# Optimization experiments

Measured on AMD Instinct MI355X. Metric: run time of the kernel, lower is better.

The kernel has to match this reference:

```python
import jax, jax.numpy as jnp
import numpy as np

SP, WD, H, HID = 8, 3, 8, 256
D = HID // H
TEMP = 0.1


def setup_inputs() -> dict:
    key = jax.random.key(0)
    ks = jax.random.split(key, 14)
    B, Lq, Lk, F = 4, 1024, 2048, SP + WD
    s = 0.05
    return {
        "q_fp": jax.random.normal(ks[0], (B, Lq, F), jnp.float32),
        "v_ret": jax.random.normal(ks[1], (B, Lk, F), jnp.float32),
        "pi_star": jax.random.uniform(ks[2], (B, Lq, Lk), jnp.float32),
        "Wq_s": jax.random.normal(ks[3], (HID, SP), jnp.float32) * s,
        "bq_s": jax.random.normal(ks[4], (HID,), jnp.float32) * s,
        "Wk_s": jax.random.normal(ks[5], (HID, SP), jnp.float32) * s,
        "bk_s": jax.random.normal(ks[6], (HID,), jnp.float32) * s,
        "Wq_w": jax.random.normal(ks[7], (HID, WD), jnp.float32) * s,
        "bq_w": jax.random.normal(ks[8], (HID,), jnp.float32) * s,
        "Wk_w": jax.random.normal(ks[9], (HID, WD), jnp.float32) * s,
        "bk_w": jax.random.normal(ks[10], (HID,), jnp.float32) * s,
        "Wv": jax.random.normal(ks[11], (HID, F), jnp.float32) * s,
        "bv": jnp.zeros((HID,), jnp.float32),
        "Wo": jax.random.normal(ks[12], (HID, HID), jnp.float32) * s,
        "bo": jnp.zeros((HID,), jnp.float32),
        "wave_blend": jnp.array(0.5, jnp.float32),
    }


def _proj(x, W, b):
    # x: [B, L, F_in] -> [B, H, L, D]
    B, L, _ = x.shape
    return (x @ W.T + b).reshape(B, L, H, D).transpose(0, 2, 1, 3)


def reference(q_fp, v_ret, pi_star, Wq_s, bq_s, Wk_s, bk_s, Wq_w, bq_w, Wk_w, bk_w, Wv, bv, Wo, bo, wave_blend):
    B, Lq, _ = q_fp.shape
    # split streams: first SP dims spatial, next WD dims wave (F == SP+WD)
    q_sp, q_wv = q_fp[..., :SP], q_fp[..., SP:SP + WD]
    k_sp, k_wv = v_ret[..., :SP], v_ret[..., SP:SP + WD]
    # structural branch: scaled dot product
    q_struct = _proj(q_sp, Wq_s, bq_s)
    k_struct = _proj(k_sp, Wk_s, bk_s)
    spatial_logits = jnp.einsum('bhqd,bhkd->bhqk', q_struct, k_struct) / np.float32(np.sqrt(D))
    # wave branch: negative squared euclidean distance via norm expansion
    q_wp = _proj(q_wv, Wq_w, bq_w)
    k_wp = _proj(k_wv, Wk_w, bk_w)
    qn = jnp.sum(q_wp * q_wp, axis=-1)[..., :, None]   # [B,H,Lq,1]
    kn = jnp.sum(k_wp * k_wp, axis=-1)[..., None, :]   # [B,H,1,Lk]
    qk = jnp.einsum('bhqd,bhkd->bhqk', q_wp, k_wp)
    wave_logits = -(qn + kn - 2.0 * qk) / np.float32(TEMP)
    alpha = jax.nn.sigmoid(wave_blend)
    transport_mask = jnp.log(jnp.clip(pi_star, 1e-9, None))[:, None]  # [B,1,Lq,Lk]
    attn = jax.nn.softmax((1.0 - alpha) * spatial_logits + alpha * wave_logits + transport_mask, axis=-1)
    values = _proj(v_ret, Wv, bv)  # [B,H,Lk,D]
    ctx = jnp.einsum('bhqk,bhkd->bhqd', attn, values)
    ctx = ctx.transpose(0, 2, 1, 3).reshape(B, Lq, HID)
    return ctx @ Wo.T + bo
```

## Files before the change

### kernel.cpp

```cpp
#include <hip/hip_runtime.h>
#include <hip/hip_bf16.h>
#include <cstdint>

#define B_    4
#define LQ    1024
#define LK    2048
#define FEAT  11
#define SP_   8
#define WD_   3
#define H_    8
#define HID_  256
#define LOG2E 1.4426950408889634f
#define SPLIT 2
#define KPS   (LK / SPLIT)
#define ITERS (KPS / 64)

typedef __attribute__((ext_vector_type(4))) float f32x4;
typedef __attribute__((ext_vector_type(8))) short bf16x8;

__device__ __forceinline__ float sigmoidf_(float x) { return 1.f / (1.f + __expf(-x)); }

__device__ __forceinline__ short f2bf(float f) {
  unsigned u = __float_as_uint(f);
  u += 0x7fffu + ((u >> 16) & 1u);
  return (short)(u >> 16);
}

__device__ __forceinline__ void gl_lds16(const void* g, void* l) {
  __builtin_amdgcn_global_load_lds(
      (const __attribute__((address_space(1))) unsigned int*)g,
      (__attribute__((address_space(3))) unsigned int*)l, 16, 0, 0);
}

__global__ __launch_bounds__(256) void proj_q_kernel(
    const float* __restrict__ q_fp, const float* __restrict__ Wq_s,
    const float* __restrict__ bq_s, const float* __restrict__ Wq_w,
    const float* __restrict__ bq_w, const float* __restrict__ wb,
    short* __restrict__ Qh)
{
  const int row = blockIdx.x;
  const int t   = threadIdx.x;
  const float alpha = sigmoidf_(wb[0]);
  const float c1 = (1.f - alpha) * 0.17677669529663687f * LOG2E;
  const float c2 = 2.f * alpha * 10.f * LOG2E;

  const float* x = q_fp + (size_t)row * FEAT;
  float xs[FEAT];
  #pragma unroll
  for (int f = 0; f < FEAT; ++f) xs[f] = x[f];

  float s = bq_s[t];
  #pragma unroll
  for (int f = 0; f < SP_; ++f) s += xs[f] * Wq_s[t * SP_ + f];
  float w = bq_w[t];
  #pragma unroll
  for (int f = 0; f < WD_; ++f) w += xs[SP_ + f] * Wq_w[t * WD_ + f];

  const int h = t >> 5, d = t & 31;
  const int b = row >> 10, q = row & (LQ - 1);
  const size_t base = ((size_t)(b * H_ + h) * LQ + q) * 64;
  Qh[base + d]      = f2bf(c1 * s);
  Qh[base + 32 + d] = f2bf(c2 * w);
}

__global__ __launch_bounds__(256) void projk_pack_kernel(
    const float* __restrict__ v_ret, const float* __restrict__ Wk_s,
    const float* __restrict__ bk_s, const float* __restrict__ Wk_w,
    const float* __restrict__ bk_w, const float* __restrict__ Wv,
    const float* __restrict__ bv,   const float* __restrict__ wb,
    short* __restrict__ KV, float* __restrict__ kb)
{
  __shared__ float ldsv[64][33];
  const int blk = blockIdx.x, bh = blockIdx.y;
  const int b = bh >> 3, h = bh & 7;
  const int t = threadIdx.x;
  const int kl = t >> 2, part = t & 3;
  const int k = blk * 64 + kl;
  const float alpha = sigmoidf_(wb[0]);

  const float* x = v_ret + (size_t)(b * LK + k) * FEAT;
  float xs[FEAT];
  #pragma unroll
  for (int f = 0; f < FEAT; ++f) xs[f] = x[f];

  float s8[8], w8[8], v8[8];
  #pragma unroll
  for (int i = 0; i < 8; ++i) {
    const int d = h * 32 + part * 8 + i;
    float s = bk_s[d];
    #pragma unroll
    for (int f = 0; f < SP_; ++f) s += xs[f] * Wk_s[d * SP_ + f];
    float w = bk_w[d];
    #pragma unroll
    for (int f = 0; f < WD_; ++f) w += xs[SP_ + f] * Wk_w[d * WD_ + f];
    float v = bv[d];
    #pragma unroll
    for (int f = 0; f < FEAT; ++f) v += xs[f] * Wv[d * FEAT + f];
    s8[i] = s; w8[i] = w; v8[i] = v;
    ldsv[kl][part * 8 + i] = v;
  }

  float sq = 0.f;
  #pragma unroll
  for (int i = 0; i < 8; ++i) sq += w8[i] * w8[i];
  sq += __shfl_xor(sq, 1);
  sq += __shfl_xor(sq, 2);
  if (part == 0) kb[(size_t)bh * LK + k] = -10.f * alpha * LOG2E * sq;

  const int a  = kl >> 5;
  const int bb = (kl >> 2) & 1;
  const int p  = kl - a * 32 - bb * 4;
  const int lo = ((p >> 3) << 2) | (p & 3);
  const int t4 = a * 2 + bb;
  const size_t base = ((size_t)bh * 32 + blk) * 768;

  bf16x8 hs, hw;
  #pragma unroll
  for (int i = 0; i < 8; ++i) { hs[i] = f2bf(s8[i]); hw[i] = f2bf(w8[i]); }
  *(bf16x8*)(KV + (base + (t4 * 2 + 0) * 64 + part * 16 + lo) * 8) = hs;
  *(bf16x8*)(KV + (base + (t4 * 2 + 1) * 64 + part * 16 + lo) * 8) = hw;

  __syncthreads();

  {
    const int j = t >> 6, l = t & 63;
    const int dt = j >> 1, kw = j & 1;
    const int lo2 = l & 15, quad = l >> 4;
    const int d = dt * 16 + lo2;
    bf16x8 hv;
    #pragma unroll
    for (int i = 0; i < 8; ++i)
      hv[i] = f2bf(ldsv[kw * 32 + quad * 8 + i][d]);
    *(bf16x8*)(KV + (base + 512 + t) * 8) = hv;
  }
}

__global__ __launch_bounds__(256) void pi_prepack_kernel(
    const float* __restrict__ pi, float* __restrict__ piP)
{
  const int Gid = blockIdx.x * 256 + threadIdx.x;
  const int g    = Gid & 255;
  const int kblk = (Gid >> 8) & 31;
  const int qt   = (Gid >> 13) & 63;
  const int b    = Gid >> 19;
  const int t4 = g >> 6, l = g & 63;
  const int lo = l & 15, quad = l >> 4;
  const int q = qt * 16 + lo;
  const int k = kblk * 64 + ((t4 >> 1) << 5) + ((t4 & 1) << 2) + quad * 8;
  const f32x4 v = *(const f32x4*)(pi + ((size_t)(b * LQ + q) * LK + k));
  *(f32x4*)(piP + (size_t)Gid * 4) = v;
}

union PF { int i[4]; bf16x8 v; };

__global__ __launch_bounds__(256, 4) void attn_kernel(
    const short* __restrict__ Qh, const short* __restrict__ KV,
    const float* __restrict__ kb, const float* __restrict__ piP,
    float* __restrict__ part)
{
  __shared__ short skv[2][6144];
  const int bh = blockIdx.y;
  const int sp = blockIdx.z;
  const int b = bh >> 3;
  const int wv = threadIdx.x >> 6;
  const int lane = threadIdx.x & 63;
  const int lo16 = lane & 15;
  const int quad = lane >> 4;
  const int q = blockIdx.x * 64 + wv * 16 + lo16;
  const int qt = blockIdx.x * 4 + wv;
  const int k0 = sp * KPS;
  const int blk0 = sp * 16;

  const size_t qoff = ((size_t)bh * LQ + q) * 64 + quad * 8;
  const bf16x8 qh0 = *(const bf16x8*)(Qh + qoff);
  const bf16x8 qh1 = *(const bf16x8*)(Qh + qoff + 32);

  const float* pibase = piP + (((size_t)(b * 64 + qt) * 32 + blk0) << 10) + lane * 4;
  const float* kbbase = kb + (size_t)bh * LK + k0 + quad * 8;

  float m = -1e30f, l = 0.f;
  f32x4 o0 = {0.f, 0.f, 0.f, 0.f}, o1 = {0.f, 0.f, 0.f, 0.f};

  {
    const size_t gb = ((size_t)bh * 32 + blk0) * 768;
    #pragma unroll
    for (int c = 0; c < 3; ++c)
      gl_lds16(KV + (gb + c * 256 + wv * 64 + lane) * 8,
               &skv[0][c * 2048 + wv * 512]);
  }

  #pragma unroll 2
  for (int it = 0; it < ITERS; ++it) {
    __syncthreads();
    if (it + 1 < ITERS) {
      const size_t gb = ((size_t)bh * 32 + blk0 + it + 1) * 768;
      short* db = skv[(it + 1) & 1];
      #pragma unroll
      for (int c = 0; c < 3; ++c)
        gl_lds16(KV + (gb + c * 256 + wv * 64 + lane) * 8,
                 db + c * 2048 + wv * 512);
    }
    const short* cbuf = skv[it & 1];

    const float* pp = pibase + (it << 10);
    f32x4 pi4[4];
    #pragma unroll
    for (int t4 = 0; t4 < 4; ++t4) pi4[t4] = *(const f32x4*)(pp + t4 * 256);
    const float* bp = kbbase + it * 64;
    f32x4 kb4[4];
    kb4[0] = *(const f32x4*)(bp);      kb4[1] = *(const f32x4*)(bp + 4);
    kb4[2] = *(const f32x4*)(bp + 32); kb4[3] = *(const f32x4*)(bp + 36);

    f32x4 st[4];
    #pragma unroll
    for (int t4 = 0; t4 < 4; ++t4) {
      const bf16x8 ka0 = *(const bf16x8*)(cbuf + ((t4 * 2 + 0) * 64 + lane) * 8);
      const bf16x8 ka1 = *(const bf16x8*)(cbuf + ((t4 * 2 + 1) * 64 + lane) * 8);
      f32x4 z = {0.f, 0.f, 0.f, 0.f};
      z = __builtin_amdgcn_mfma_f32_16x16x32_bf16(ka0, qh0, z, 0, 0, 0);
      z = __builtin_amdgcn_mfma_f32_16x16x32_bf16(ka1, qh1, z, 0, 0, 0);
      st[t4] = z;
    }

    float lg[16];
    #pragma unroll
    for (int t4 = 0; t4 < 4; ++t4) {
      #pragma unroll
      for (int r = 0; r < 4; ++r) lg[t4 * 4 + r] = st[t4][r] + kb4[t4][r];
    }

    float cm = lg[0];
    #pragma unroll
    for (int j = 1; j < 16; ++j) cm = fmaxf(cm, lg[j]);
    cm = fmaxf(cm, __shfl_xor(cm, 16));
    cm = fmaxf(cm, __shfl_xor(cm, 32));
    const float mn = fmaxf(m, cm);
    const float sc = __builtin_amdgcn_exp2f(m - mn);

    unsigned eu[16];
    #pragma unroll
    for (int t4 = 0; t4 < 4; ++t4) {
      #pragma unroll
      for (int r = 0; r < 4; ++r)
        eu[t4 * 4 + r] = __float_as_uint(
            __builtin_amdgcn_exp2f(lg[t4 * 4 + r] - mn) * fmaxf(pi4[t4][r], 1e-9f));
    }

    PF pf0, pf1;
    float ps = 0.f;
    #pragma unroll
    for (int p = 0; p < 4; ++p) {
      const int w0 = __builtin_amdgcn_perm(eu[2 * p + 1], eu[2 * p], 0x07060302u);
      const int w1 = __builtin_amdgcn_perm(eu[8 + 2 * p + 1], eu[8 + 2 * p], 0x07060302u);
      pf0.i[p] = w0; pf1.i[p] = w1;
      ps += __uint_as_float(((unsigned)w0) << 16) + __uint_as_float(w0 & 0xffff0000u);
      ps += __uint_as_float(((unsigned)w1) << 16) + __uint_as_float(w1 & 0xffff0000u);
    }
    ps += __shfl_xor(ps, 16);
    ps += __shfl_xor(ps, 32);
    l = l * sc + ps;
    m = mn;
    #pragma unroll
    for (int r = 0; r < 4; ++r) { o0[r] *= sc; o1[r] *= sc; }

    const bf16x8 va00 = *(const bf16x8*)(cbuf + ((512 + 0 * 64) + lane) * 8);
    const bf16x8 va01 = *(const bf16x8*)(cbuf + ((512 + 1 * 64) + lane) * 8);
    const bf16x8 va10 = *(const bf16x8*)(cbuf + ((512 + 2 * 64) + lane) * 8);
    const bf16x8 va11 = *(const bf16x8*)(cbuf + ((512 + 3 * 64) + lane) * 8);
    o0 = __builtin_amdgcn_mfma_f32_16x16x32_bf16(va00, pf0.v, o0, 0, 0, 0);
    o0 = __builtin_amdgcn_mfma_f32_16x16x32_bf16(va01, pf1.v, o0, 0, 0, 0);
    o1 = __builtin_amdgcn_mfma_f32_16x16x32_bf16(va10, pf0.v, o1, 0, 0, 0);
    o1 = __builtin_amdgcn_mfma_f32_16x16x32_bf16(va11, pf1.v, o1, 0, 0, 0);
  }

  float* ppart = part + ((size_t)(sp * 32 + bh) * LQ + q) * 36;
  if (quad == 0) { ppart[0] = m; ppart[1] = l; }
  *(f32x4*)(ppart + 4 + quad * 4)  = o0;
  *(f32x4*)(ppart + 20 + quad * 4) = o1;
}

__global__ __launch_bounds__(256) void out_kernel(
    const float* __restrict__ part, const float* __restrict__ Wo,
    const float* __restrict__ bo, float* __restrict__ out)
{
  __shared__ float cs[16 * 256];
  const int t = threadIdx.x;
  const size_t r0 = (size_t)blockIdx.x * 16;

  {
    const int col4 = (t & 63) * 4;
    const int h = col4 >> 5, d = col4 & 31;
    #pragma unroll
    for (int i = 0; i < 4; ++i) {
      const int row = i * 4 + (t >> 6);
      const size_t gq = r0 + row;
      const int b = (int)(gq >> 10), qq = (int)(gq & (LQ - 1));
      const size_t r = ((size_t)(b * H_ + h) * LQ + qq);
      const float* p0 = part + r * 36;
      const float* p1 = part + (r + (size_t)B_ * H_ * LQ) * 36;
      const float m0 = p0[0], l0 = p0[1], m1 = p1[0], l1 = p1[1];
      const float mM = fmaxf(m0, m1);
      const float w0 = __builtin_amdgcn_exp2f(m0 - mM);
      const float w1 = __builtin_amdgcn_exp2f(m1 - mM);
      const float inv = 1.f / (w0 * l0 + w1 * l1);
      const f32x4 a0 = *(const f32x4*)(p0 + 4 + d);
      const f32x4 a1 = *(const f32x4*)(p1 + 4 + d);
      f32x4 cv;
      #pragma unroll
      for (int j = 0; j < 4; ++j) cv[j] = (w0 * a0[j] + w1 * a1[j]) * inv;
      *(f32x4*)(cs + row * 256 + col4) = cv;
    }
  }
  __syncthreads();

  const int o0 = (t & 63) * 4;
  const int rs = (t >> 6) * 4;
  float acc[4][4];
  #pragma unroll
  for (int r = 0; r < 4; ++r) {
    #pragma unroll
    for (int j = 0; j < 4; ++j) acc[r][j] = bo[o0 + j];
  }

  for (int c4 = 0; c4 < 64; ++c4) {
    const f32x4 w0 = *(const f32x4*)(Wo + (size_t)(o0 + 0) * HID_ + c4 * 4);
    const f32x4 w1 = *(const f32x4*)(Wo + (size_t)(o0 + 1) * HID_ + c4 * 4);
    const f32x4 w2 = *(const f32x4*)(Wo + (size_t)(o0 + 2) * HID_ + c4 * 4);
    const f32x4 w3 = *(const f32x4*)(Wo + (size_t)(o0 + 3) * HID_ + c4 * 4);
    #pragma unroll
    for (int r = 0; r < 4; ++r) {
      const f32x4 cv = *(const f32x4*)(cs + (rs + r) * 256 + c4 * 4);
      acc[r][0] += cv[0] * w0[0] + cv[1] * w0[1] + cv[2] * w0[2] + cv[3] * w0[3];
      acc[r][1] += cv[0] * w1[0] + cv[1] * w1[1] + cv[2] * w1[2] + cv[3] * w1[3];
      acc[r][2] += cv[0] * w2[0] + cv[1] * w2[1] + cv[2] * w2[2] + cv[3] * w2[3];
      acc[r][3] += cv[0] * w3[0] + cv[1] * w3[1] + cv[2] * w3[2] + cv[3] * w3[3];
    }
  }
  #pragma unroll
  for (int r = 0; r < 4; ++r) {
    f32x4 res;
    res[0] = acc[r][0]; res[1] = acc[r][1]; res[2] = acc[r][2]; res[3] = acc[r][3];
    *(f32x4*)(out + (r0 + rs + r) * HID_ + o0) = res;
  }
}

extern "C" void kernel_launch(void* const* d_in, const int* in_sizes, int n_in,
                              void* d_out, int out_size, void* d_ws, size_t ws_size,
                              hipStream_t stream)
{
  const float* q_fp  = (const float*)d_in[0];
  const float* v_ret = (const float*)d_in[1];
  const float* pi    = (const float*)d_in[2];
  const float* Wq_s  = (const float*)d_in[3];
  const float* bq_s  = (const float*)d_in[4];
  const float* Wk_s  = (const float*)d_in[5];
  const float* bk_s  = (const float*)d_in[6];
  const float* Wq_w  = (const float*)d_in[7];
  const float* bq_w  = (const float*)d_in[8];
  const float* Wk_w  = (const float*)d_in[9];
  const float* bk_w  = (const float*)d_in[10];
  const float* Wv    = (const float*)d_in[11];
  const float* bv    = (const float*)d_in[12];
  const float* Wo    = (const float*)d_in[13];
  const float* bo    = (const float*)d_in[14];
  const float* wb    = (const float*)d_in[15];
  float* out = (float*)d_out;

  short* Qh   = (short*)d_ws;
  short* KV   = Qh + (size_t)2097152;
  float* kbuf = (float*)(KV + (size_t)6291456);
  float* piP  = kbuf + (size_t)65536;
  float* part = piP + (size_t)8388608;

  proj_q_kernel<<<B_ * LQ, 256, 0, stream>>>(q_fp, Wq_s, bq_s, Wq_w, bq_w, wb, Qh);
  projk_pack_kernel<<<dim3(LK / 64, 32), 256, 0, stream>>>(
      v_ret, Wk_s, bk_s, Wk_w, bk_w, Wv, bv, wb, KV, kbuf);
  pi_prepack_kernel<<<8192, 256, 0, stream>>>(pi, piP);
  attn_kernel<<<dim3(LQ / 64, 32, SPLIT), 256, 0, stream>>>(Qh, KV, kbuf, piP, part);
  out_kernel<<<(B_ * LQ) / 16, 256, 0, stream>>>(part, Wo, bo, out);
}
```

Before: 205.2 us.

## Compute output projection with split-bf16 MFMA instead of scalar FP32 FMAs

```diff
diff --git a/kernel.cpp b/kernel.cpp
--- a/kernel.cpp
+++ b/kernel.cpp
@@ -17,6 +17,7 @@
 
 typedef __attribute__((ext_vector_type(4))) float f32x4;
 typedef __attribute__((ext_vector_type(8))) short bf16x8;
+typedef __attribute__((ext_vector_type(4))) short s16x4;
 
 __device__ __forceinline__ float sigmoidf_(float x) { return 1.f / (1.f + __expf(-x)); }
 
@@ -24,6 +25,9 @@
   unsigned u = __float_as_uint(f);
   u += 0x7fffu + ((u >> 16) & 1u);
   return (short)(u >> 16);
+}
+__device__ __forceinline__ float bf2f(short s) {
+  return __uint_as_float(((unsigned)(unsigned short)s) << 16);
 }
 
 __device__ __forceinline__ void gl_lds16(const void* g, void* l) {
@@ -279,68 +283,81 @@
   *(f32x4*)(ppart + 20 + quad * 4) = o1;
 }
 
+__global__ __launch_bounds__(256) void wo_prep_kernel(
+    const float* __restrict__ Wo, short* __restrict__ WoH, short* __restrict__ WoL)
+{
+  const int i = (blockIdx.x * 256 + threadIdx.x) * 4;
+  const f32x4 v = *(const f32x4*)(Wo + i);
+  s16x4 h, l;
+  #pragma unroll
+  for (int j = 0; j < 4; ++j) {
+    h[j] = f2bf(v[j]);
+    l[j] = f2bf(v[j] - bf2f(h[j]));
+  }
+  *(s16x4*)(WoH + i) = h;
+  *(s16x4*)(WoL + i) = l;
+}
+
 __global__ __launch_bounds__(256) void out_kernel(
-    const float* __restrict__ part, const float* __restrict__ Wo,
-    const float* __restrict__ bo, float* __restrict__ out)
-{
-  __shared__ float cs[16 * 256];
+    const float* __restrict__ part, const short* __restrict__ WoH,
+    const short* __restrict__ WoL, const float* __restrict__ bo,
+    float* __restrict__ out)
+{
   const int t = threadIdx.x;
-  const size_t r0 = (size_t)blockIdx.x * 16;
-
-  {
-    const int col4 = (t & 63) * 4;
-    const int h = col4 >> 5, d = col4 & 31;
-    #pragma unroll
-    for (int i = 0; i < 4; ++i) {
-      const int row = i * 4 + (t >> 6);
-      const size_t gq = r0 + row;
-      const int b = (int)(gq >> 10), qq = (int)(gq & (LQ - 1));
-      const size_t r = ((size_t)(b * H_ + h) * LQ + qq);
-      const float* p0 = part + r * 36;
-      const float* p1 = part + (r + (size_t)B_ * H_ * LQ) * 36;
-      const float m0 = p0[0], l0 = p0[1], m1 = p1[0], l1 = p1[1];
-      const float mM = fmaxf(m0, m1);
-      const float w0 = __builtin_amdgcn_exp2f(m0 - mM);
-      const float w1 = __builtin_amdgcn_exp2f(m1 - mM);
-      const float inv = 1.f / (w0 * l0 + w1 * l1);
-      const f32x4 a0 = *(const f32x4*)(p0 + 4 + d);
-      const f32x4 a1 = *(const f32x4*)(p1 + 4 + d);
-      f32x4 cv;
-      #pragma unroll
-      for (int j = 0; j < 4; ++j) cv[j] = (w0 * a0[j] + w1 * a1[j]) * inv;
-      *(f32x4*)(cs + row * 256 + col4) = cv;
-    }
-  }
-  __syncthreads();
-
-  const int o0 = (t & 63) * 4;
-  const int rs = (t >> 6) * 4;
-  float acc[4][4];
-  #pragma unroll
-  for (int r = 0; r < 4; ++r) {
-    #pragma unroll
-    for (int j = 0; j < 4; ++j) acc[r][j] = bo[o0 + j];
-  }
-
-  for (int c4 = 0; c4 < 64; ++c4) {
-    const f32x4 w0 = *(const f32x4*)(Wo + (size_t)(o0 + 0) * HID_ + c4 * 4);
-    const f32x4 w1 = *(const f32x4*)(Wo + (size_t)(o0 + 1) * HID_ + c4 * 4);
-    const f32x4 w2 = *(const f32x4*)(Wo + (size_t)(o0 + 2) * HID_ + c4 * 4);
-    const f32x4 w3 = *(const f32x4*)(Wo + (size_t)(o0 + 3) * HID_ + c4 * 4);
-    #pragma unroll
-    for (int r = 0; r < 4; ++r) {
-      const f32x4 cv = *(const f32x4*)(cs + (rs + r) * 256 + c4 * 4);
-      acc[r][0] += cv[0] * w0[0] + cv[1] * w0[1] + cv[2] * w0[2] + cv[3] * w0[3];
-      acc[r][1] += cv[0] * w1[0] + cv[1] * w1[1] + cv[2] * w1[2] + cv[3] * w1[3];
-      acc[r][2] += cv[0] * w2[0] + cv[1] * w2[1] + cv[2] * w2[2] + cv[3] * w2[3];
-      acc[r][3] += cv[0] * w3[0] + cv[1] * w3[1] + cv[2] * w3[2] + cv[3] * w3[3];
-    }
-  }
-  #pragma unroll
-  for (int r = 0; r < 4; ++r) {
-    f32x4 res;
-    res[0] = acc[r][0]; res[1] = acc[r][1]; res[2] = acc[r][2]; res[3] = acc[r][3];
-    *(f32x4*)(out + (r0 + rs + r) * HID_ + o0) = res;
+  const int wv = t >> 6, lane = t & 63;
+  const int lo16 = lane & 15, quad = lane >> 4;
+  const int mt = blockIdx.x;
+  const size_t gq = (size_t)mt * 16 + lo16;
+  const int b = (int)(gq >> 10), qq = (int)(gq & (LQ - 1));
+
+  bf16x8 Ah[8], Al[8];
+  #pragma unroll
+  for (int win = 0; win < 8; ++win) {
+    const size_t r = (size_t)(b * H_ + win) * LQ + qq;
+    const float* p0 = part + r * 36;
+    const float* p1 = part + (r + (size_t)B_ * H_ * LQ) * 36;
+    const float m0 = p0[0], l0 = p0[1], m1 = p1[0], l1 = p1[1];
+    const float mM = fmaxf(m0, m1);
+    const float w0 = __builtin_amdgcn_exp2f(m0 - mM);
+    const float w1 = __builtin_amdgcn_exp2f(m1 - mM);
+    const float inv = 1.f / (w0 * l0 + w1 * l1);
+    const f32x4 a0  = *(const f32x4*)(p0 + 4 + quad * 8);
+    const f32x4 a0b = *(const f32x4*)(p0 + 8 + quad * 8);
+    const f32x4 a1  = *(const f32x4*)(p1 + 4 + quad * 8);
+    const f32x4 a1b = *(const f32x4*)(p1 + 8 + quad * 8);
+    float c8[8];
+    #pragma unroll
+    for (int j = 0; j < 4; ++j) {
+      c8[j]     = (w0 * a0[j]  + w1 * a1[j])  * inv;
+      c8[4 + j] = (w0 * a0b[j] + w1 * a1b[j]) * inv;
+    }
+    #pragma unroll
+    for (int j = 0; j < 8; ++j) {
+      const short hi = f2bf(c8[j]);
+      Ah[win][j] = hi;
+      Al[win][j] = f2bf(c8[j] - bf2f(hi));
+    }
+  }
+
+  const int n0 = wv * 64;
+  #pragma unroll
+  for (int nt = 0; nt < 4; ++nt) {
+    const int nb = n0 + nt * 16;
+    const short* bh = WoH + (size_t)(nb + lo16) * HID_ + quad * 8;
+    const short* bl = WoL + (size_t)(nb + lo16) * HID_ + quad * 8;
+    const float bias = bo[nb + lo16];
+    f32x4 acc = {bias, bias, bias, bias};
+    #pragma unroll
+    for (int win = 0; win < 8; ++win) {
+      const bf16x8 Bh = *(const bf16x8*)(bh + win * 32);
+      const bf16x8 Bl = *(const bf16x8*)(bl + win * 32);
+      acc = __builtin_amdgcn_mfma_f32_16x16x32_bf16(Ah[win], Bh, acc, 0, 0, 0);
+      acc = __builtin_amdgcn_mfma_f32_16x16x32_bf16(Al[win], Bh, acc, 0, 0, 0);
+      acc = __builtin_amdgcn_mfma_f32_16x16x32_bf16(Ah[win], Bl, acc, 0, 0, 0);
+    }
+    #pragma unroll
+    for (int r4 = 0; r4 < 4; ++r4)
+      out[(size_t)(mt * 16 + quad * 4 + r4) * HID_ + nb + lo16] = acc[r4];
   }
 }
 
@@ -371,11 +388,14 @@
   float* kbuf = (float*)(KV + (size_t)6291456);
   float* piP  = kbuf + (size_t)65536;
   float* part = piP + (size_t)8388608;
+  short* WoH  = (short*)piP;
+  short* WoL  = WoH + (size_t)65536;
 
   proj_q_kernel<<<B_ * LQ, 256, 0, stream>>>(q_fp, Wq_s, bq_s, Wq_w, bq_w, wb, Qh);
   projk_pack_kernel<<<dim3(LK / 64, 32), 256, 0, stream>>>(
       v_ret, Wk_s, bk_s, Wk_w, bk_w, Wv, bv, wb, KV, kbuf);
   pi_prepack_kernel<<<8192, 256, 0, stream>>>(pi, piP);
   attn_kernel<<<dim3(LQ / 64, 32, SPLIT), 256, 0, stream>>>(Qh, KV, kbuf, piP, part);
-  out_kernel<<<(B_ * LQ) / 16, 256, 0, stream>>>(part, Wo, bo, out);
-}
+  wo_prep_kernel<<<64, 256, 0, stream>>>(Wo, WoH, WoL);
+  out_kernel<<<(B_ * LQ) / 16, 256, 0, stream>>>(part, WoH, WoL, bo, out);
+}
```

Result: faster. 179.1 us (-12.8%).
